# Kernel optimization log

Measured on AMD Instinct MI355X. Metric: run time of the kernel, lower is better.

Reference implementation:

```python
import jax, jax.numpy as jnp
import numpy as np

C = 256          # conv_channels
C1 = C // 2      # 128
C2 = C // 4      # 64
G = 1            # relation_glimpse


def setup_inputs() -> dict:
    key = jax.random.key(0)
    ks = jax.random.split(key, 20)
    bs, Nr, in_dim, q_dim = 4, 256, 2052, 1024
    d_in = in_dim + 4  # pos (first 4 coords) re-appended
    s = 0.02
    inp = {
        "Q": jax.random.normal(ks[0], (bs, q_dim), jnp.float32),
        "X": jax.random.normal(ks[1], (bs, Nr, in_dim), jnp.float32),
        "Wv": jax.random.normal(ks[2], (d_in, C), jnp.float32) * s,
        "bv": jnp.zeros((C,), jnp.float32),
        "Wq": jax.random.normal(ks[3], (q_dim, C), jnp.float32) * s,
        "bq": jnp.zeros((C,), jnp.float32),
        # branch 0 (r_conv01/02/03): 1x1 convs == per-position dense
        "W01": jax.random.normal(ks[4], (C, C1), jnp.float32) * s,
        "b01": jnp.zeros((C1,), jnp.float32),
        "W02": jax.random.normal(ks[5], (C1, C2), jnp.float32) * s,
        "b02": jnp.zeros((C2,), jnp.float32),
        "W03": jax.random.normal(ks[6], (C2, G), jnp.float32) * s,
        "b03": jnp.zeros((G,), jnp.float32),
        # branch 1 (r_conv1/2/3): dilation on 1x1 kernels is a no-op
        "W1": jax.random.normal(ks[7], (C, C1), jnp.float32) * s,
        "b1": jnp.zeros((C1,), jnp.float32),
        "W2": jax.random.normal(ks[8], (C1, C2), jnp.float32) * s,
        "b2": jnp.zeros((C2,), jnp.float32),
        "W3": jax.random.normal(ks[9], (C2, G), jnp.float32) * s,
        "b3": jnp.zeros((G,), jnp.float32),
    }
    return inp


def _mlp3(P, Wa, ba, Wb, bb, Wc, bc):
    # P: [bs, Nr, Nr, C]; three 1x1-conv layers, ReLU after each (incl. last).
    h = jax.nn.relu(jnp.einsum("bijc,ck->bijk", P, Wa) + ba)
    h = jax.nn.relu(jnp.einsum("bijc,ck->bijk", h, Wb) + bb)
    h = jax.nn.relu(jnp.einsum("bijc,ck->bijk", h, Wc) + bc)
    return h[..., 0]  # [bs, Nr, Nr] (relation_glimpse == 1)


def _attn_map(h):
    # symmetrize, then softmax over all Nr*Nr positions
    s = h + jnp.swapaxes(h, 1, 2)
    bs, Nr, _ = s.shape
    return jax.nn.softmax(s.reshape(bs, Nr * Nr), axis=-1).reshape(bs, Nr, Nr)


def reference(Q, X, Wv, bv, Wq, bq, W01, b01, W02, b02, W03, b03,
              W1, b1, W2, b2, W3, b3):
    X_ = X
    # append pos (first 4 coords) -> [bs, Nr, in_dim+4]
    Xcat = jnp.concatenate([X, X[:, :, :4]], axis=2)
    Xp = jnp.einsum("bnd,dc->bnc", Xcat, Wv) + bv
    Qp = Q @ Wq + bq
    Xp = Xp + Qp[:, None, :]                       # [bs, Nr, C]
    P = Xp[:, None, :, :] * Xp[:, :, None, :]      # [bs, Nr, Nr, C] pairwise product
    m0 = _attn_map(_mlp3(P, W01, b01, W02, b02, W03, b03))
    m1 = _attn_map(_mlp3(P, W1, b1, W2, b2, W3, b3))
    # weighted aggregation with original features; /(2*glimpse), then sum over Nr
    rel = jnp.einsum("bij,bjd->bid", m0 + m1, X_) / (2.0 * G)
    return rel.sum(axis=1)  # [bs, in_dim]
```

## Files before the change

### kernel.cpp

```cpp
#include <hip/hip_runtime.h>
#include <hip/hip_bf16.h>

typedef __attribute__((ext_vector_type(8)))  short short8;
typedef __attribute__((ext_vector_type(4)))  float f32x4;
typedef __attribute__((ext_vector_type(16))) float f32x16;

#define NR 256
#define CC 256

__device__ __forceinline__ unsigned short f2bf(float x) {
    union { float f; unsigned int u; } v; v.f = x;
    unsigned int r = v.u + 0x7FFFu + ((v.u >> 16) & 1u);
    return (unsigned short)(r >> 16);
}

__device__ __forceinline__ unsigned int pk2bf(float a, float b) {
    __hip_bfloat162 h = __float22bfloat162_rn(make_float2(a, b));
    union { __hip_bfloat162 h; unsigned int u; } cv; cv.h = h;
    return cv.u;
}

__global__ __launch_bounds__(256) void setup_kernel(
    const float* __restrict__ Q, const float* __restrict__ Wq, float* __restrict__ Qpp,
    const float* __restrict__ Wv, unsigned short* __restrict__ wvp,
    const float* __restrict__ W01, const float* __restrict__ W1,
    const float* __restrict__ W02, const float* __restrict__ W2,
    unsigned short* __restrict__ wpa, unsigned short* __restrict__ wpb)
{
    __shared__ float tile[32][260];
    __shared__ float qs[256];
    const int bx = blockIdx.x;
    const int tid = threadIdx.x;

    if (bx < 16) {
        int ksl = bx & 3, b = bx >> 2;
        qs[tid] = Q[b * 1024 + ksl * 256 + tid];
        __syncthreads();
        float acc = 0.f;
        #pragma unroll 4
        for (int d = 0; d < 256; ++d) acc += qs[d] * Wq[(size_t)(ksl * 256 + d) * 256 + tid];
        Qpp[(ksl * 4 + b) * 256 + tid] = acc;
    } else if (bx < 81) {
        int ks = bx - 16;
        for (int idx = tid; idx < 32 * 256; idx += 256) {
            int cr = idx >> 8, n = idx & 255;
            int c = ks * 32 + cr;
            tile[cr][n] = (c < 2056) ? Wv[(size_t)c * 256 + n] : 0.f;
        }
        __syncthreads();
        #pragma unroll
        for (int q = 0; q < 4; ++q) {
            int t2 = tid * 4 + q;
            int nt = t2 >> 6, l = t2 & 63;
            int gg = l >> 4, jj = l & 15;
            short8 s;
            #pragma unroll
            for (int e = 0; e < 8; ++e)
                s[e] = (short)f2bf(tile[gg * 8 + e][nt * 16 + jj]);
            *(short8*)&wvp[((size_t)(ks * 16 + nt) * 64 + l) * 8] = s;
        }
    } else {
        int t = (bx - 81) * 256 + tid;
        if (t < 65536) {
            int e = t & 7, l = (t >> 3) & 63, ks = (t >> 9) & 15, nt = (t >> 13) & 3, br = (t >> 15) & 1;
            int cc = ks * 16 + (l >> 5) * 8 + e;
            int n = nt * 32 + (l & 31);
            const float* W = br ? W1 : W01;
            wpa[t] = f2bf(W[cc * 128 + n]);
        } else {
            int t2 = t - 65536;
            int e = t2 & 7, l = (t2 >> 3) & 63, ks = (t2 >> 9) & 7, nt = (t2 >> 12) & 1, br = (t2 >> 13) & 1;
            int cc = ks * 16 + (l >> 5) * 8 + e;
            int n = nt * 32 + (l & 31);
            const float* W = br ? W2 : W02;
            wpb[t2] = f2bf(W[cc * 64 + n]);
        }
    }
}

__global__ __launch_bounds__(512) void xp_kernel(
    const float* __restrict__ X, const unsigned short* __restrict__ wvp,
    const float* __restrict__ bv, const float* __restrict__ bq,
    const float* __restrict__ Qpp, float* __restrict__ Xp)
{
    __shared__ f32x4 red[8][2][65];
    const int tid = threadIdx.x;
    const int w = tid >> 6;
    const int lane = tid & 63;
    const int g = lane >> 4, j16 = lane & 15;
    const int mt = blockIdx.x;
    const int bn = blockIdx.y;
    const int b  = blockIdx.z;

    const int i0 = mt * 16;
    const int n0 = bn * 32;
    const float* xrow = X + ((size_t)(b * NR) + (i0 + j16)) * 2052;

    f32x4 acc[2] = {};

    for (int ks = w; ks < 64; ks += 8) {
        const int c0 = ks * 32 + g * 8;
        float4 xa = *(const float4*)(xrow + c0);
        float4 xb = *(const float4*)(xrow + c0 + 4);
        union { short8 s; unsigned int u[4]; } af;
        af.u[0] = pk2bf(xa.x, xa.y);
        af.u[1] = pk2bf(xa.z, xa.w);
        af.u[2] = pk2bf(xb.x, xb.y);
        af.u[3] = pk2bf(xb.z, xb.w);
        #pragma unroll
        for (int nt = 0; nt < 2; ++nt) {
            short8 bf = ((const short8*)wvp)[(size_t)(ks * 16 + bn * 2 + nt) * 64 + lane];
            acc[nt] = __builtin_amdgcn_mfma_f32_16x16x32_bf16(af.s, bf, acc[nt], 0, 0, 0);
        }
    }
    if (w == 0) {
        float xv[8];
        #pragma unroll
        for (int e = 0; e < 8; ++e) {
            int q = g * 8 + e;
            int csrc = (q < 4) ? (2048 + q) : (q - 4);
            xv[e] = xrow[csrc];
        }
        union { short8 s; unsigned int u[4]; } af;
        af.u[0] = pk2bf(xv[0], xv[1]);
        af.u[1] = pk2bf(xv[2], xv[3]);
        af.u[2] = pk2bf(xv[4], xv[5]);
        af.u[3] = pk2bf(xv[6], xv[7]);
        #pragma unroll
        for (int nt = 0; nt < 2; ++nt) {
            short8 bf = ((const short8*)wvp)[(size_t)(64 * 16 + bn * 2 + nt) * 64 + lane];
            acc[nt] = __builtin_amdgcn_mfma_f32_16x16x32_bf16(af.s, bf, acc[nt], 0, 0, 0);
        }
    }
    #pragma unroll
    for (int nt = 0; nt < 2; ++nt) red[w][nt][lane] = acc[nt];
    __syncthreads();

    {
        int nt  = tid >> 8;
        int rem = tid & 255;
        int l   = rem & 63;
        int reg = (rem >> 6) & 3;
        float r = 0.f;
        #pragma unroll
        for (int ww = 0; ww < 8; ++ww) r += red[ww][nt][l][reg];
        int gg = l >> 4, jj = l & 15;
        int n = n0 + nt * 16 + jj;
        float base = bv[n] + bq[n] + Qpp[b * 256 + n] + Qpp[(4 + b) * 256 + n]
                   + Qpp[(8 + b) * 256 + n] + Qpp[(12 + b) * 256 + n];
        int row = i0 + gg * 4 + reg;
        Xp[((b * NR) + row) * CC + n] = r + base;
    }
}

__global__ __launch_bounds__(512, 2) void pairs_kernel(
    const float* __restrict__ Xp,
    const unsigned short* __restrict__ wpa,
    const unsigned short* __restrict__ wpb,
    const float* __restrict__ b01, const float* __restrict__ b02,
    const float* __restrict__ b03,
    const float* __restrict__ b1,  const float* __restrict__ b2,
    const float* __restrict__ b3,
    const float* __restrict__ W03, const float* __restrict__ W3,
    float* __restrict__ colpart, float* __restrict__ rowpart)
{
    __shared__ __align__(16) unsigned short lds_wa[32768];
    __shared__ __align__(16) float lds_si[2048];
    __shared__ __align__(16) float lds_bias1[128];
    __shared__ __align__(16) float lds_bias2[64];
    __shared__ __align__(16) float lds_w3[64];
    __shared__ float lds_c[8][33];

    const int tid = threadIdx.x;
    const int wave = tid >> 6;
    const int lane = tid & 63;
    const int hi = lane >> 5;
    const int j32 = lane & 31;

    int bx = blockIdx.x;
    int b = bx / 288;
    int r = bx - b * 288;
    int br = r / 144;
    int u = r - br * 144;
    int k = 0, off = 0;
    while (k < 7) {
        int cnt = 4 * (8 - k);
        if (u < off + cnt) break;
        off += cnt; ++k;
    }
    int rel = u - off;
    int it8 = 4 * k + rel / (8 - k);
    int jt  = k + rel % (8 - k);

    const int i = it8 * 8 + wave;
    const int blk = br * 4 + b;
    const int j0 = jt * 32;
    const int j = j0 + j32;

    *(float4*)&lds_si[wave * 256 + lane * 4] =
        *(const float4*)&Xp[((b * NR) + i) * CC + lane * 4];

    {
        const uint4* g1 = (const uint4*)(wpa + (size_t)br * 32768);
        uint4* s1 = (uint4*)lds_wa;
        #pragma unroll
        for (int kk = 0; kk < 8; ++kk) s1[kk * 512 + tid] = g1[kk * 512 + tid];
        if (tid < 128) lds_bias1[tid] = br ? b1[tid] : b01[tid];
        else if (tid < 192) lds_bias2[tid - 128] = br ? b2[tid - 128] : b02[tid - 128];
        else if (tid < 256) lds_w3[tid - 192] = br ? W3[tid - 192] : W03[tid - 192];
    }
    __syncthreads();
    const float b3v = br ? b3[0] : b03[0];
    const float* si = lds_si + wave * 256;

    const float* xr = Xp + ((size_t)(b * NR) + j) * CC;
    short8 bfr[16];
    #pragma unroll
    for (int ks = 0; ks < 16; ++ks) {
        const int c0 = ks * 16 + hi * 8;
        float4 xa = *(const float4*)(xr + c0);
        float4 xb = *(const float4*)(xr + c0 + 4);
        float4 sa = *(const float4*)(si + c0);
        float4 sb = *(const float4*)(si + c0 + 4);
        union { short8 s; unsigned int uu[4]; } f;
        f.uu[0] = pk2bf(xa.x * sa.x, xa.y * sa.y);
        f.uu[1] = pk2bf(xa.z * sa.z, xa.w * sa.w);
        f.uu[2] = pk2bf(xb.x * sb.x, xb.y * sb.y);
        f.uu[3] = pk2bf(xb.z * sb.z, xb.w * sb.w);
        bfr[ks] = f.s;
    }

    f32x16 acc1[4];
    #pragma unroll
    for (int t = 0; t < 4; ++t) {
        #pragma unroll
        for (int q = 0; q < 4; ++q) {
            const float* bb = &lds_bias1[t * 32 + q * 8 + hi * 4];
            acc1[t][q * 4 + 0] = bb[0];
            acc1[t][q * 4 + 1] = bb[1];
            acc1[t][q * 4 + 2] = bb[2];
            acc1[t][q * 4 + 3] = bb[3];
        }
    }
    #pragma unroll
    for (int ks = 0; ks < 16; ++ks) {
        const short8 bb = bfr[ks];
        #pragma unroll
        for (int t = 0; t < 4; ++t) {
            short8 wf = ((const short8*)lds_wa)[(t * 16 + ks) * 64 + lane];
            acc1[t] = __builtin_amdgcn_mfma_f32_32x32x16_bf16(wf, bb, acc1[t], 0, 0, 0);
        }
    }

    short8 w2r[16];
    {
        const short8* wb = (const short8*)wpb + (size_t)br * 1024;
        #pragma unroll
        for (int q = 0; q < 16; ++q) w2r[q] = wb[q * 64 + lane];
    }

    f32x16 acc2[2];
    #pragma unroll
    for (int nt = 0; nt < 2; ++nt) {
        #pragma unroll
        for (int q = 0; q < 4; ++q) {
            const float* bb = &lds_bias2[nt * 32 + q * 8 + hi * 4];
            acc2[nt][q * 4 + 0] = bb[0];
            acc2[nt][q * 4 + 1] = bb[1];
            acc2[nt][q * 4 + 2] = bb[2];
            acc2[nt][q * 4 + 3] = bb[3];
        }
    }
    #pragma unroll
    for (int t = 0; t < 4; ++t) {
        #pragma unroll
        for (int s = 0; s < 2; ++s) {
            const int bse = s * 8;
            float rA0 = fmaxf(acc1[t][bse + 0], 0.f), rA1 = fmaxf(acc1[t][bse + 1], 0.f);
            float rA2 = fmaxf(acc1[t][bse + 2], 0.f), rA3 = fmaxf(acc1[t][bse + 3], 0.f);
            float rB0 = fmaxf(acc1[t][bse + 4], 0.f), rB1 = fmaxf(acc1[t][bse + 5], 0.f);
            float rB2 = fmaxf(acc1[t][bse + 6], 0.f), rB3 = fmaxf(acc1[t][bse + 7], 0.f);
            unsigned int uA0 = pk2bf(rA0, rA1), uA1 = pk2bf(rA2, rA3);
            unsigned int uB0 = pk2bf(rB0, rB1), uB1 = pk2bf(rB2, rB3);
            unsigned int pA0 = __shfl_xor(uA0, 32, 64), pA1 = __shfl_xor(uA1, 32, 64);
            unsigned int pB0 = __shfl_xor(uB0, 32, 64), pB1 = __shfl_xor(uB1, 32, 64);
            union { short8 s8; unsigned int uu[4]; } B2;
            B2.uu[0] = hi ? pB0 : uA0;
            B2.uu[1] = hi ? pB1 : uA1;
            B2.uu[2] = hi ? uB0 : pA0;
            B2.uu[3] = hi ? uB1 : pA1;
            const int ks2 = 2 * t + s;
            acc2[0] = __builtin_amdgcn_mfma_f32_32x32x16_bf16(w2r[ks2], B2.s8, acc2[0], 0, 0, 0);
            acc2[1] = __builtin_amdgcn_mfma_f32_32x32x16_bf16(w2r[8 + ks2], B2.s8, acc2[1], 0, 0, 0);
        }
    }

    float part = 0.f;
    #pragma unroll
    for (int nt = 0; nt < 2; ++nt) {
        #pragma unroll
        for (int q = 0; q < 4; ++q) {
            const float* wv = &lds_w3[nt * 32 + q * 8 + hi * 4];
            part += fmaxf(acc2[nt][q * 4 + 0], 0.f) * wv[0];
            part += fmaxf(acc2[nt][q * 4 + 1], 0.f) * wv[1];
            part += fmaxf(acc2[nt][q * 4 + 2], 0.f) * wv[2];
            part += fmaxf(acc2[nt][q * 4 + 3], 0.f) * wv[3];
        }
    }
    part += __shfl_xor(part, 32, 64);
    const float h3 = fmaxf(part + b3v, 0.f);
    const float E = __expf(2.f * h3);
    const float Ec = (j >= i) ? E : 0.f;
    float Er = (j >  i) ? E : 0.f;

    Er += __shfl_xor(Er, 1, 64);
    Er += __shfl_xor(Er, 2, 64);
    Er += __shfl_xor(Er, 4, 64);
    Er += __shfl_xor(Er, 8, 64);
    Er += __shfl_xor(Er, 16, 64);
    Er += __shfl_xor(Er, 32, 64);
    if (lane == 0)
        rowpart[((size_t)blk * NR + i) * 8 + jt] = 0.5f * Er;

    if (!hi) lds_c[wave][j32] = Ec;
    __syncthreads();
    if (tid < 32) {
        float c = 0.f;
        #pragma unroll
        for (int w2 = 0; w2 < 8; ++w2) c += lds_c[w2][tid];
        colpart[(size_t)blk * 4608 + 64 * jt * (jt + 1) + tid * (4 * jt + 4) + it8] = c;
    }
}

__global__ __launch_bounds__(256) void colsoft_final_kernel(
    const float* __restrict__ colpart, const float* __restrict__ rowpart,
    float* __restrict__ wn)
{
    const int blk = blockIdx.x;
    const int j = threadIdx.x;
    const int jt = j >> 5, j32l = j & 31;
    const int cnt = 4 * jt + 4;
    float cs = 0.f;
    const float* cp = colpart + (size_t)blk * 4608 + 64 * jt * (jt + 1) + j32l * cnt;
    for (int it2 = 0; it2 < cnt; ++it2) cs += cp[it2];
    const float* rp = rowpart + ((size_t)blk * NR + j) * 8;
    for (int q = jt; q < 8; ++q) cs += rp[q];

    __shared__ float red[256];
    red[j] = cs; __syncthreads();
    for (int s = 128; s > 0; s >>= 1) {
        if (j < s) red[j] += red[j + s];
        __syncthreads();
    }
    wn[blk * 256 + j] = cs / red[0];
}

__global__ __launch_bounds__(256) void agg_part_kernel(
    const float* __restrict__ X, const float* __restrict__ wn,
    float* __restrict__ apart)
{
    const int dc = blockIdx.x, b = blockIdx.y, jc = blockIdx.z;
    const int d = dc * 256 + threadIdx.x;
    __shared__ float wc[32];
    if (threadIdx.x < 32) {
        int j = jc * 32 + threadIdx.x;
        wc[threadIdx.x] = 0.5f * (wn[b * 256 + j] + wn[(4 + b) * 256 + j]);
    }
    __syncthreads();
    if (d < 2052) {
        const float* xp = X + (size_t)b * NR * 2052 + (size_t)jc * 32 * 2052 + d;
        float a0 = 0.f, a1 = 0.f, a2 = 0.f, a3 = 0.f;
        for (int rr = 0; rr < 32; rr += 4) {
            a0 += wc[rr + 0] * xp[(size_t)(rr + 0) * 2052];
            a1 += wc[rr + 1] * xp[(size_t)(rr + 1) * 2052];
            a2 += wc[rr + 2] * xp[(size_t)(rr + 2) * 2052];
            a3 += wc[rr + 3] * xp[(size_t)(rr + 3) * 2052];
        }
        apart[(size_t)(jc * 4 + b) * 2304 + d] = (a0 + a1) + (a2 + a3);
    }
}

__global__ __launch_bounds__(256) void agg_final_kernel(
    const float* __restrict__ apart, float* __restrict__ out)
{
    const int dc = blockIdx.x, b = blockIdx.y;
    const int d = dc * 256 + threadIdx.x;
    if (d < 2052) {
        float s = 0.f;
        #pragma unroll
        for (int jc = 0; jc < 8; ++jc) s += apart[(size_t)(jc * 4 + b) * 2304 + d];
        out[b * 2052 + d] = s;
    }
}

extern "C" void kernel_launch(void* const* d_in, const int* in_sizes, int n_in,
                              void* d_out, int out_size, void* d_ws, size_t ws_size,
                              hipStream_t stream) {
    const float* Q   = (const float*)d_in[0];
    const float* X   = (const float*)d_in[1];
    const float* Wv  = (const float*)d_in[2];
    const float* bv  = (const float*)d_in[3];
    const float* Wq  = (const float*)d_in[4];
    const float* bq  = (const float*)d_in[5];
    const float* W01 = (const float*)d_in[6];
    const float* b01 = (const float*)d_in[7];
    const float* W02 = (const float*)d_in[8];
    const float* b02 = (const float*)d_in[9];
    const float* W03 = (const float*)d_in[10];
    const float* b03 = (const float*)d_in[11];
    const float* W1  = (const float*)d_in[12];
    const float* b1  = (const float*)d_in[13];
    const float* W2  = (const float*)d_in[14];
    const float* b2  = (const float*)d_in[15];
    const float* W3  = (const float*)d_in[16];
    const float* b3  = (const float*)d_in[17];

    char* ws = (char*)d_ws;
    float* Xp   = (float*)(ws + 0);
    float* Qpp  = (float*)(ws + 1048576);
    float* wn   = (float*)(ws + 1064960);
    unsigned short* wpa = (unsigned short*)(ws + 1073152);
    unsigned short* wpb = (unsigned short*)(ws + 1204224);
    float* colpart = (float*)(ws + 1236992);
    float* rowpart = (float*)(ws + 1384448);
    unsigned short* wvp = (unsigned short*)(ws + 1236992);
    float* apart = (float*)(ws + 0);
    float* out = (float*)d_out;

    setup_kernel<<<401, 256, 0, stream>>>(Q, Wq, Qpp, Wv, wvp,
                                          W01, W1, W02, W2, wpa, wpb);
    xp_kernel<<<dim3(16, 8, 4), 512, 0, stream>>>(X, wvp, bv, bq, Qpp, Xp);
    pairs_kernel<<<1152, 512, 0, stream>>>(Xp, wpa, wpb, b01, b02, b03,
                                           b1, b2, b3, W03, W3, colpart, rowpart);
    colsoft_final_kernel<<<8, 256, 0, stream>>>(colpart, rowpart, wn);
    agg_part_kernel<<<dim3(9, 4, 8), 256, 0, stream>>>(X, wn, apart);
    agg_final_kernel<<<dim3(9, 4), 256, 0, stream>>>(apart, out);
}
```

Before: 91.93 us.

## Split pairs-kernel K loop to cut registers, fuse softmax norm into aggregation

The pairs kernel now builds and consumes its bf16 pair fragments and second-layer weights in two halves, which lowers peak register pressure and may avoid spills at 2 blocks per CU. The xp kernel computes 64 output columns per block instead of 32, halving the grid and the repeated X reads. The separate column-softmax normalisation kernel is removed and folded into each aggregation block, which saves a launch but repeats the reduction in every block.

```diff
diff --git a/kernel.cpp b/kernel.cpp
--- a/kernel.cpp
+++ b/kernel.cpp
@@ -83,20 +83,19 @@
     const float* __restrict__ bv, const float* __restrict__ bq,
     const float* __restrict__ Qpp, float* __restrict__ Xp)
 {
-    __shared__ f32x4 red[8][2][65];
+    __shared__ f32x4 red[8][4][65];
     const int tid = threadIdx.x;
     const int w = tid >> 6;
     const int lane = tid & 63;
-    const int g = lane >> 4, j16 = lane & 15;
+    const int g = lane >> 4, j16v = lane & 15;
     const int mt = blockIdx.x;
     const int bn = blockIdx.y;
     const int b  = blockIdx.z;
 
     const int i0 = mt * 16;
-    const int n0 = bn * 32;
-    const float* xrow = X + ((size_t)(b * NR) + (i0 + j16)) * 2052;
-
-    f32x4 acc[2] = {};
+    const float* xrow = X + ((size_t)(b * NR) + (i0 + j16v)) * 2052;
+
+    f32x4 acc[4] = {};
 
     for (int ks = w; ks < 64; ks += 8) {
         const int c0 = ks * 32 + g * 8;
@@ -108,8 +107,8 @@
         af.u[2] = pk2bf(xb.x, xb.y);
         af.u[3] = pk2bf(xb.z, xb.w);
         #pragma unroll
-        for (int nt = 0; nt < 2; ++nt) {
-            short8 bf = ((const short8*)wvp)[(size_t)(ks * 16 + bn * 2 + nt) * 64 + lane];
+        for (int nt = 0; nt < 4; ++nt) {
+            short8 bf = ((const short8*)wvp)[(size_t)(ks * 16 + bn * 4 + nt) * 64 + lane];
             acc[nt] = __builtin_amdgcn_mfma_f32_16x16x32_bf16(af.s, bf, acc[nt], 0, 0, 0);
         }
     }
@@ -127,29 +126,28 @@
         af.u[2] = pk2bf(xv[4], xv[5]);
         af.u[3] = pk2bf(xv[6], xv[7]);
         #pragma unroll
-        for (int nt = 0; nt < 2; ++nt) {
-            short8 bf = ((const short8*)wvp)[(size_t)(64 * 16 + bn * 2 + nt) * 64 + lane];
+        for (int nt = 0; nt < 4; ++nt) {
+            short8 bf = ((const short8*)wvp)[(size_t)(64 * 16 + bn * 4 + nt) * 64 + lane];
             acc[nt] = __builtin_amdgcn_mfma_f32_16x16x32_bf16(af.s, bf, acc[nt], 0, 0, 0);
         }
     }
     #pragma unroll
-    for (int nt = 0; nt < 2; ++nt) red[w][nt][lane] = acc[nt];
+    for (int nt = 0; nt < 4; ++nt) red[w][nt][lane] = acc[nt];
     __syncthreads();
 
-    {
-        int nt  = tid >> 8;
-        int rem = tid & 255;
-        int l   = rem & 63;
-        int reg = (rem >> 6) & 3;
-        float r = 0.f;
-        #pragma unroll
-        for (int ww = 0; ww < 8; ++ww) r += red[ww][nt][l][reg];
+    #pragma unroll
+    for (int idx = tid; idx < 1024; idx += 512) {
+        int nt = idx >> 8, rem = idx & 255;
+        int l = rem & 63, reg = rem >> 6;
+        float rsum = 0.f;
+        #pragma unroll
+        for (int ww = 0; ww < 8; ++ww) rsum += red[ww][nt][l][reg];
         int gg = l >> 4, jj = l & 15;
-        int n = n0 + nt * 16 + jj;
+        int n = bn * 64 + nt * 16 + jj;
         float base = bv[n] + bq[n] + Qpp[b * 256 + n] + Qpp[(4 + b) * 256 + n]
                    + Qpp[(8 + b) * 256 + n] + Qpp[(12 + b) * 256 + n];
         int row = i0 + gg * 4 + reg;
-        Xp[((b * NR) + row) * CC + n] = r + base;
+        Xp[((b * NR) + row) * CC + n] = rsum + base;
     }
 }
 
@@ -212,12 +210,25 @@
     __syncthreads();
     const float b3v = br ? b3[0] : b03[0];
     const float* si = lds_si + wave * 256;
-
     const float* xr = Xp + ((size_t)(b * NR) + j) * CC;
-    short8 bfr[16];
-    #pragma unroll
-    for (int ks = 0; ks < 16; ++ks) {
-        const int c0 = ks * 16 + hi * 8;
+
+    f32x16 acc1[4];
+    #pragma unroll
+    for (int t = 0; t < 4; ++t) {
+        #pragma unroll
+        for (int q = 0; q < 4; ++q) {
+            const float* bb = &lds_bias1[t * 32 + q * 8 + hi * 4];
+            acc1[t][q * 4 + 0] = bb[0];
+            acc1[t][q * 4 + 1] = bb[1];
+            acc1[t][q * 4 + 2] = bb[2];
+            acc1[t][q * 4 + 3] = bb[3];
+        }
+    }
+
+    short8 bfr[8];
+    #pragma unroll
+    for (int ksl = 0; ksl < 8; ++ksl) {
+        const int c0 = ksl * 16 + hi * 8;
         float4 xa = *(const float4*)(xr + c0);
         float4 xb = *(const float4*)(xr + c0 + 4);
         float4 sa = *(const float4*)(si + c0);
@@ -227,36 +238,40 @@
         f.uu[1] = pk2bf(xa.z * sa.z, xa.w * sa.w);
         f.uu[2] = pk2bf(xb.x * sb.x, xb.y * sb.y);
         f.uu[3] = pk2bf(xb.z * sb.z, xb.w * sb.w);
-        bfr[ks] = f.s;
-    }
-
-    f32x16 acc1[4];
-    #pragma unroll
-    for (int t = 0; t < 4; ++t) {
-        #pragma unroll
-        for (int q = 0; q < 4; ++q) {
-            const float* bb = &lds_bias1[t * 32 + q * 8 + hi * 4];
-            acc1[t][q * 4 + 0] = bb[0];
-            acc1[t][q * 4 + 1] = bb[1];
-            acc1[t][q * 4 + 2] = bb[2];
-            acc1[t][q * 4 + 3] = bb[3];
-        }
-    }
-    #pragma unroll
-    for (int ks = 0; ks < 16; ++ks) {
-        const short8 bb = bfr[ks];
+        bfr[ksl] = f.s;
+    }
+    #pragma unroll
+    for (int ksl = 0; ksl < 8; ++ksl) {
+        const short8 bb = bfr[ksl];
         #pragma unroll
         for (int t = 0; t < 4; ++t) {
-            short8 wf = ((const short8*)lds_wa)[(t * 16 + ks) * 64 + lane];
+            short8 wf = ((const short8*)lds_wa)[(t * 16 + ksl) * 64 + lane];
             acc1[t] = __builtin_amdgcn_mfma_f32_32x32x16_bf16(wf, bb, acc1[t], 0, 0, 0);
         }
     }
 
-    short8 w2r[16];
-    {
-        const short8* wb = (const short8*)wpb + (size_t)br * 1024;
-        #pragma unroll
-        for (int q = 0; q < 16; ++q) w2r[q] = wb[q * 64 + lane];
+    #pragma unroll
+    for (int ksl = 0; ksl < 8; ++ksl) {
+        const int c0 = (8 + ksl) * 16 + hi * 8;
+        float4 xa = *(const float4*)(xr + c0);
+        float4 xb = *(const float4*)(xr + c0 + 4);
+        float4 sa = *(const float4*)(si + c0);
+        float4 sb = *(const float4*)(si + c0 + 4);
+        union { short8 s; unsigned int uu[4]; } f;
+        f.uu[0] = pk2bf(xa.x * sa.x, xa.y * sa.y);
+        f.uu[1] = pk2bf(xa.z * sa.z, xa.w * sa.w);
+        f.uu[2] = pk2bf(xb.x * sb.x, xb.y * sb.y);
+        f.uu[3] = pk2bf(xb.z * sb.z, xb.w * sb.w);
+        bfr[ksl] = f.s;
+    }
+    #pragma unroll
+    for (int ksl = 0; ksl < 8; ++ksl) {
+        const short8 bb = bfr[ksl];
+        #pragma unroll
+        for (int t = 0; t < 4; ++t) {
+            short8 wf = ((const short8*)lds_wa)[(t * 16 + 8 + ksl) * 64 + lane];
+            acc1[t] = __builtin_amdgcn_mfma_f32_32x32x16_bf16(wf, bb, acc1[t], 0, 0, 0);
+        }
     }
 
     f32x16 acc2[2];
@@ -271,8 +286,16 @@
             acc2[nt][q * 4 + 3] = bb[3];
         }
     }
-    #pragma unroll
-    for (int t = 0; t < 4; ++t) {
+    const short8* wb = (const short8*)wpb + (size_t)br * 1024;
+
+    short8 w2r[8];
+    #pragma unroll
+    for (int q = 0; q < 4; ++q) {
+        w2r[q]     = wb[q * 64 + lane];
+        w2r[4 + q] = wb[(8 + q) * 64 + lane];
+    }
+    #pragma unroll
+    for (int t = 0; t < 2; ++t) {
         #pragma unroll
         for (int s = 0; s < 2; ++s) {
             const int bse = s * 8;
@@ -291,7 +314,35 @@
             B2.uu[3] = hi ? uB1 : pA1;
             const int ks2 = 2 * t + s;
             acc2[0] = __builtin_amdgcn_mfma_f32_32x32x16_bf16(w2r[ks2], B2.s8, acc2[0], 0, 0, 0);
-            acc2[1] = __builtin_amdgcn_mfma_f32_32x32x16_bf16(w2r[8 + ks2], B2.s8, acc2[1], 0, 0, 0);
+            acc2[1] = __builtin_amdgcn_mfma_f32_32x32x16_bf16(w2r[4 + ks2], B2.s8, acc2[1], 0, 0, 0);
+        }
+    }
+    #pragma unroll
+    for (int q = 0; q < 4; ++q) {
+        w2r[q]     = wb[(4 + q) * 64 + lane];
+        w2r[4 + q] = wb[(12 + q) * 64 + lane];
+    }
+    #pragma unroll
+    for (int t = 2; t < 4; ++t) {
+        #pragma unroll
+        for (int s = 0; s < 2; ++s) {
+            const int bse = s * 8;
+            float rA0 = fmaxf(acc1[t][bse + 0], 0.f), rA1 = fmaxf(acc1[t][bse + 1], 0.f);
+            float rA2 = fmaxf(acc1[t][bse + 2], 0.f), rA3 = fmaxf(acc1[t][bse + 3], 0.f);
+            float rB0 = fmaxf(acc1[t][bse + 4], 0.f), rB1 = fmaxf(acc1[t][bse + 5], 0.f);
+            float rB2 = fmaxf(acc1[t][bse + 6], 0.f), rB3 = fmaxf(acc1[t][bse + 7], 0.f);
+            unsigned int uA0 = pk2bf(rA0, rA1), uA1 = pk2bf(rA2, rA3);
+            unsigned int uB0 = pk2bf(rB0, rB1), uB1 = pk2bf(rB2, rB3);
+            unsigned int pA0 = __shfl_xor(uA0, 32, 64), pA1 = __shfl_xor(uA1, 32, 64);
+            unsigned int pB0 = __shfl_xor(uB0, 32, 64), pB1 = __shfl_xor(uB1, 32, 64);
+            union { short8 s8; unsigned int uu[4]; } B2;
+            B2.uu[0] = hi ? pB0 : uA0;
+            B2.uu[1] = hi ? pB1 : uA1;
+            B2.uu[2] = hi ? uB0 : pA0;
+            B2.uu[3] = hi ? uB1 : pA1;
+            const int ks2 = 2 * t + s - 4;
+            acc2[0] = __builtin_amdgcn_mfma_f32_32x32x16_bf16(w2r[ks2], B2.s8, acc2[0], 0, 0, 0);
+            acc2[1] = __builtin_amdgcn_mfma_f32_32x32x16_bf16(w2r[4 + ks2], B2.s8, acc2[1], 0, 0, 0);
         }
     }
 
@@ -327,46 +378,48 @@
     if (tid < 32) {
         float c = 0.f;
         #pragma unroll
-        for (int w2 = 0; w2 < 8; ++w2) c += lds_c[w2][tid];
+        for (int wv2 = 0; wv2 < 8; ++wv2) c += lds_c[wv2][tid];
         colpart[(size_t)blk * 4608 + 64 * jt * (jt + 1) + tid * (4 * jt + 4) + it8] = c;
     }
 }
 
-__global__ __launch_bounds__(256) void colsoft_final_kernel(
-    const float* __restrict__ colpart, const float* __restrict__ rowpart,
-    float* __restrict__ wn)
-{
-    const int blk = blockIdx.x;
-    const int j = threadIdx.x;
-    const int jt = j >> 5, j32l = j & 31;
-    const int cnt = 4 * jt + 4;
-    float cs = 0.f;
-    const float* cp = colpart + (size_t)blk * 4608 + 64 * jt * (jt + 1) + j32l * cnt;
-    for (int it2 = 0; it2 < cnt; ++it2) cs += cp[it2];
-    const float* rp = rowpart + ((size_t)blk * NR + j) * 8;
-    for (int q = jt; q < 8; ++q) cs += rp[q];
-
-    __shared__ float red[256];
-    red[j] = cs; __syncthreads();
-    for (int s = 128; s > 0; s >>= 1) {
-        if (j < s) red[j] += red[j + s];
-        __syncthreads();
-    }
-    wn[blk * 256 + j] = cs / red[0];
-}
-
 __global__ __launch_bounds__(256) void agg_part_kernel(
-    const float* __restrict__ X, const float* __restrict__ wn,
-    float* __restrict__ apart)
+    const float* __restrict__ X, const float* __restrict__ colpart,
+    const float* __restrict__ rowpart, float* __restrict__ apart)
 {
     const int dc = blockIdx.x, b = blockIdx.y, jc = blockIdx.z;
-    const int d = dc * 256 + threadIdx.x;
+    const int tid = threadIdx.x;
+    __shared__ float csh[2][256];
+    __shared__ float red2[2][256];
     __shared__ float wc[32];
-    if (threadIdx.x < 32) {
-        int j = jc * 32 + threadIdx.x;
-        wc[threadIdx.x] = 0.5f * (wn[b * 256 + j] + wn[(4 + b) * 256 + j]);
+
+    {
+        const int jt = tid >> 5, j32l = tid & 31;
+        const int cnt = 4 * jt + 4;
+        #pragma unroll
+        for (int brx = 0; brx < 2; ++brx) {
+            const int blk = brx * 4 + b;
+            float cs = 0.f;
+            const float* cp = colpart + (size_t)blk * 4608 + 64 * jt * (jt + 1) + j32l * cnt;
+            for (int it2 = 0; it2 < cnt; ++it2) cs += cp[it2];
+            const float* rp = rowpart + ((size_t)blk * NR + tid) * 8;
+            for (int q = jt; q < 8; ++q) cs += rp[q];
+            csh[brx][tid] = cs;
+            red2[brx][tid] = cs;
+        }
     }
     __syncthreads();
+    for (int s = 128; s > 0; s >>= 1) {
+        if (tid < s) { red2[0][tid] += red2[0][tid + s]; red2[1][tid] += red2[1][tid + s]; }
+        __syncthreads();
+    }
+    if (tid < 32) {
+        int jx = jc * 32 + tid;
+        wc[tid] = 0.5f * (csh[0][jx] / red2[0][0] + csh[1][jx] / red2[1][0]);
+    }
+    __syncthreads();
+
+    const int d = dc * 256 + tid;
     if (d < 2052) {
         const float* xp = X + (size_t)b * NR * 2052 + (size_t)jc * 32 * 2052 + d;
         float a0 = 0.f, a1 = 0.f, a2 = 0.f, a3 = 0.f;
@@ -418,7 +471,6 @@
     char* ws = (char*)d_ws;
     float* Xp   = (float*)(ws + 0);
     float* Qpp  = (float*)(ws + 1048576);
-    float* wn   = (float*)(ws + 1064960);
     unsigned short* wpa = (unsigned short*)(ws + 1073152);
     unsigned short* wpb = (unsigned short*)(ws + 1204224);
     float* colpart = (float*)(ws + 1236992);
@@ -429,10 +481,9 @@
 
     setup_kernel<<<401, 256, 0, stream>>>(Q, Wq, Qpp, Wv, wvp,
                                           W01, W1, W02, W2, wpa, wpb);
-    xp_kernel<<<dim3(16, 8, 4), 512, 0, stream>>>(X, wvp, bv, bq, Qpp, Xp);
+    xp_kernel<<<dim3(16, 4, 4), 512, 0, stream>>>(X, wvp, bv, bq, Qpp, Xp);
     pairs_kernel<<<1152, 512, 0, stream>>>(Xp, wpa, wpb, b01, b02, b03,
                                            b1, b2, b3, W03, W3, colpart, rowpart);
-    colsoft_final_kernel<<<8, 256, 0, stream>>>(colpart, rowpart, wn);
-    agg_part_kernel<<<dim3(9, 4, 8), 256, 0, stream>>>(X, wn, apart);
+    agg_part_kernel<<<dim3(9, 4, 8), 256, 0, stream>>>(X, colpart, rowpart, apart);
     agg_final_kernel<<<dim3(9, 4), 256, 0, stream>>>(apart, out);
 }
```

New measurement: 100.9 us. 1.1x slower.
